# Performance work log

Hardware: AMD Instinct MI355X
Metric: run time of the kernel (lower is better)

## Reference

```python
import jax, jax.numpy as jnp
from jax import lax
import numpy as np

B, C, H, W = 16, 16, 256, 256
NOISE = 4
HID = 128
CDIM = 64
NCLS = 32
STEP_SIZE = 0.1
FIN = 3 * C + NOISE  # 52


def _lin(k, fin, fout, scale=None):
    # torch nn.Linear default init: U(-1/sqrt(fin), 1/sqrt(fin))
    s = (1.0 / np.sqrt(fin)) if scale is None else scale
    kw, kb = jax.random.split(k)
    w = jax.random.uniform(kw, (fin, fout), minval=-s, maxval=s, dtype=jnp.float32)
    b = jax.random.uniform(kb, (fout,), minval=-s, maxval=s, dtype=jnp.float32)
    return w, b


def setup_inputs() -> dict:
    key = jax.random.key(0)
    ks = jax.random.split(key, 8)
    x = jax.random.normal(ks[0], (B, C, H, W), dtype=jnp.float32)
    cond = jax.random.randint(ks[1], (B,), 0, NCLS)
    embed_tab = jax.random.normal(ks[2], (NCLS, CDIM), dtype=jnp.float32)
    film1_w, film1_b = _lin(ks[3], CDIM, 2 * HID)
    film2_w, film2_b = _lin(ks[4], CDIM, 2 * HID)
    fc1_w, fc1_b = _lin(ks[5], FIN, HID)
    fc2_w, fc2_b = _lin(ks[6], HID, HID)
    # original zero-inits fc3 (degenerate); use small random instead
    fc3_w, fc3_b = _lin(ks[7], HID, C, scale=0.02)
    return dict(x=x, cond=cond, embed_tab=embed_tab,
                film1_w=film1_w, film1_b=film1_b,
                film2_w=film2_w, film2_b=film2_b,
                fc1_w=fc1_w, fc1_b=fc1_b, fc2_w=fc2_w, fc2_b=fc2_b,
                fc3_w=fc3_w, fc3_b=fc3_b, n_steps=1)


def _dwconv(v, k2d):
    # depthwise 3x3 'same' conv, NCHW / OIHW
    kern = jnp.broadcast_to(k2d, (C, 1, 3, 3)).astype(v.dtype)
    return lax.conv_general_dilated(v, kern, (1, 1), 'SAME', feature_group_count=C)


def reference(x, cond, embed_tab, film1_w, film1_b, film2_w, film2_b,
              fc1_w, fc1_b, fc2_w, fc2_b, fc3_w, fc3_b, n_steps):
    sobel_x = jnp.array([[-1., 0., 1.], [-2., 0., 2.], [-1., 0., 1.]], jnp.float32)
    sobel_y = sobel_x.T
    emb = embed_tab[cond]                       # [B, CDIM]
    f1 = emb @ film1_w + film1_b                # [B, 2*HID]
    gamma1, beta1 = f1[:, :HID], f1[:, HID:]
    f2 = emb @ film2_w + film2_b
    gamma2, beta2 = f2[:, :HID], f2[:, HID:]
    for t in range(n_steps):
        gx = _dwconv(x, sobel_x)
        gy = _dwconv(x, sobel_y)
        noise = jax.random.normal(jax.random.fold_in(jax.random.key(1), t),
                                  (B, NOISE, H, W), dtype=x.dtype)
        feats = jnp.concatenate([x, gx, gy, noise], axis=1).transpose(0, 2, 3, 1)  # [B,H,W,FIN]
        h = jax.nn.relu(feats @ fc1_w + fc1_b)
        h = gamma1[:, None, None, :] * h + beta1[:, None, None, :]
        h = jax.nn.relu(h @ fc2_w + fc2_b)
        h = gamma2[:, None, None, :] * h + beta2[:, None, None, :]
        dx = (h @ fc3_w + fc3_b).transpose(0, 3, 1, 2)  # [B,C,H,W]
        dx = jnp.clip(dx, -10.0, 10.0)
        x = x + dx * STEP_SIZE
    return x
```

## Files before the change

### kernel.cpp

```cpp
#include <hip/hip_runtime.h>
#include <hip/hip_bf16.h>

using short8 = __attribute__((ext_vector_type(8))) short;
using f32x4  = __attribute__((ext_vector_type(4))) float;

constexpr int Bn = 16, Cc = 16, Hh = 256, Ww = 256;
constexpr int NOISEC = 4, HID = 128, CDIM = 64;
constexpr unsigned NTOT = (unsigned)Bn * NOISEC * Hh * Ww;
constexpr unsigned HALF = NTOT / 2;

__host__ __device__ __forceinline__ unsigned rotl(unsigned x, int d) {
    return (x << d) | (x >> (32 - d));
}

__host__ __device__ __forceinline__ void tf2x32(unsigned k0, unsigned k1,
                                                unsigned c0, unsigned c1,
                                                unsigned& o0, unsigned& o1) {
    unsigned k2 = k0 ^ k1 ^ 0x1BD11BDAu;
    unsigned x0 = c0 + k0, x1 = c1 + k1;
    x0 += x1; x1 = rotl(x1, 13); x1 ^= x0;
    x0 += x1; x1 = rotl(x1, 15); x1 ^= x0;
    x0 += x1; x1 = rotl(x1, 26); x1 ^= x0;
    x0 += x1; x1 = rotl(x1, 6);  x1 ^= x0;
    x0 += k1; x1 += k2 + 1u;
    x0 += x1; x1 = rotl(x1, 17); x1 ^= x0;
    x0 += x1; x1 = rotl(x1, 29); x1 ^= x0;
    x0 += x1; x1 = rotl(x1, 16); x1 ^= x0;
    x0 += x1; x1 = rotl(x1, 24); x1 ^= x0;
    x0 += k2; x1 += k0 + 2u;
    x0 += x1; x1 = rotl(x1, 13); x1 ^= x0;
    x0 += x1; x1 = rotl(x1, 15); x1 ^= x0;
    x0 += x1; x1 = rotl(x1, 26); x1 ^= x0;
    x0 += x1; x1 = rotl(x1, 6);  x1 ^= x0;
    x0 += k0; x1 += k1 + 3u;
    x0 += x1; x1 = rotl(x1, 17); x1 ^= x0;
    x0 += x1; x1 = rotl(x1, 29); x1 ^= x0;
    x0 += x1; x1 = rotl(x1, 16); x1 ^= x0;
    x0 += x1; x1 = rotl(x1, 24); x1 ^= x0;
    x0 += k1; x1 += k2 + 4u;
    x0 += x1; x1 = rotl(x1, 13); x1 ^= x0;
    x0 += x1; x1 = rotl(x1, 15); x1 ^= x0;
    x0 += x1; x1 = rotl(x1, 26); x1 ^= x0;
    x0 += x1; x1 = rotl(x1, 6);  x1 ^= x0;
    x0 += k2; x1 += k0 + 5u;
    o0 = x0; o1 = x1;
}

__device__ __forceinline__ float erfinv_f(float x) {
    float w = -log1pf(-x * x);
    float p;
    if (w < 5.0f) {
        w = w - 2.5f;
        p = 2.81022636e-08f;
        p = fmaf(p, w, 3.43273939e-07f);
        p = fmaf(p, w, -3.5233877e-06f);
        p = fmaf(p, w, -4.39150654e-06f);
        p = fmaf(p, w, 0.00021858087f);
        p = fmaf(p, w, -0.00125372503f);
        p = fmaf(p, w, -0.00417768164f);
        p = fmaf(p, w, 0.246640727f);
        p = fmaf(p, w, 1.50140941f);
    } else {
        w = sqrtf(w) - 3.0f;
        p = -0.000200214257f;
        p = fmaf(p, w, 0.000100950558f);
        p = fmaf(p, w, 0.00134934322f);
        p = fmaf(p, w, -0.00367342844f);
        p = fmaf(p, w, 0.00573950773f);
        p = fmaf(p, w, -0.0076224613f);
        p = fmaf(p, w, 0.00943887047f);
        p = fmaf(p, w, 1.00167406f);
        p = fmaf(p, w, 2.83297682f);
    }
    return p * x;
}

__device__ __forceinline__ float noise_val(unsigned j, unsigned fk0, unsigned fk1) {
    unsigned i = (j < HALF) ? j : (j - HALF);
    unsigned o0, o1;
    tf2x32(fk0, fk1, i, i + HALF, o0, o1);
    unsigned bits = (j < HALF) ? o0 : o1;
    unsigned fb = (bits >> 9) | 0x3F800000u;
    float f = __uint_as_float(fb) - 1.0f;
    const float lo = -0.99999994f;
    float u = f * 2.0f + lo;
    u = fmaxf(lo, u);
    return 1.4142135381698608f * erfinv_f(u);
}

__device__ __forceinline__ ushort f2bf(float f) {
    unsigned u = __float_as_uint(f);
    unsigned r = (u + 0x7FFFu + ((u >> 16) & 1u)) >> 16;
    return (ushort)r;
}

__device__ __forceinline__ unsigned cvtpk(float lo, float hi) {
    unsigned r;
    asm volatile("v_cvt_pk_bf16_f32 %0, %1, %2" : "=v"(r) : "v"(lo), "v"(hi));
    return r;
}

__device__ __forceinline__ unsigned rsw(int row) {
    return ((unsigned)((row ^ (row >> 4)) & 15)) << 4;
}

__global__ void film_kernel(const int* __restrict__ cond,
                            const float* __restrict__ embed,
                            const float* __restrict__ f1w, const float* __restrict__ f1b,
                            const float* __restrict__ f2w, const float* __restrict__ f2b,
                            float* __restrict__ film) {
    int b = blockIdx.x;
    int j = threadIdx.x;
    __shared__ float emb[CDIM];
    if (j < CDIM) emb[j] = embed[(size_t)cond[b] * CDIM + j];
    __syncthreads();
    float a1 = f1b[j], a2 = f2b[j];
    for (int c = 0; c < CDIM; ++c) {
        float e = emb[c];
        a1 += e * f1w[c * 2 * HID + j];
        a2 += e * f2w[c * 2 * HID + j];
    }
    int which = j >> 7;
    int idx = j & 127;
    float* fb_ = film + (size_t)b * 4 * HID;
    fb_[which * HID + idx] = a1;
    fb_[(2 + which) * HID + idx] = a2;
}

__global__ void prep_weights(const float* __restrict__ fc1w,
                             const float* __restrict__ fc2w,
                             const float* __restrict__ fc3w,
                             ushort* __restrict__ w1t, ushort* __restrict__ w2t,
                             ushort* __restrict__ w3t) {
    int i = blockIdx.x * 256 + threadIdx.x;
    if (i < 128 * 64) {
        int j = i >> 6, k = i & 63;
        w1t[i] = (k < 52) ? f2bf(fc1w[k * HID + j]) : (ushort)0;
    } else if (i < 8192 + 128 * 128) {
        int m = i - 8192;
        int j = m >> 7, k = m & 127;
        w2t[m] = f2bf(fc2w[k * HID + j]);
    } else if (i < 8192 + 16384 + 16 * 128) {
        int m = i - 24576;
        int c = m >> 7, k = m & 127;
        w3t[m] = f2bf(fc3w[k * Cc + c]);
    }
}

__global__ __launch_bounds__(256, 2)
void nca_mfma(const float* __restrict__ x,
              const ushort* __restrict__ w1t, const ushort* __restrict__ w2t,
              const ushort* __restrict__ w3t,
              const float* __restrict__ fc1b, const float* __restrict__ fc2b,
              const float* __restrict__ fc3b, const float* __restrict__ film,
              float* __restrict__ out, unsigned fk0, unsigned fk1) {
    __shared__ __align__(16) unsigned char Hb[256 * 256];

    const int P = blockIdx.x;
    const int blk = ((P & 7) << 9) | (P >> 3);
    const int b = blk >> 8, y = blk & 255;
    const int t = threadIdx.x;
    const float* xb = x + (size_t)b * Cc * Hh * Ww;

    {
        const int q  = t & 63;
        const int cq = t >> 6;
        const int px0 = q * 4;
        const bool okm = (y > 0), okp = (y < Hh - 1);
        const bool ql = (q > 0), qr = (q < 63);
        const float4 fz = {0.f, 0.f, 0.f, 0.f};

        float4 RM[4], RC[4], RP[4];
        #pragma unroll
        for (int cc = 0; cc < 4; ++cc) {
            const int c = cq * 4 + cc;
            const float* base = xb + ((size_t)c * Hh + (size_t)y) * Ww + px0;
            RM[cc] = okm ? *(const float4*)(base - Ww) : fz;
            RC[cc] = *(const float4*)(base);
            RP[cc] = okp ? *(const float4*)(base + Ww) : fz;
        }

        ushort nzs[4];
        {
            unsigned nbase = (((unsigned)(b * NOISEC + cq) * Hh + (unsigned)y) * Ww)
                             + (unsigned)px0;
            #pragma unroll
            for (int i = 0; i < 4; ++i)
                nzs[i] = f2bf(noise_val(nbase + (unsigned)i, fk0, fk1));
        }
        #pragma unroll
        for (int i = 0; i < 4; ++i) {
            const int row = px0 + i;
            const unsigned sw = rsw(row);
            *(ushort*)(Hb + row * 256 + (((224u ^ sw) + 2u * cq))) = nzs[i];
        }
        if (cq == 0) {
            #pragma unroll
            for (int i = 0; i < 4; ++i) {
                const int row = px0 + i;
                const unsigned sw = rsw(row);
                *(uint2*)(Hb + row * 256 + ((232u & 15u) + (224u ^ sw))) = (uint2){0u, 0u};
                *(uint4*)(Hb + row * 256 + (240u ^ sw)) = (uint4){0u, 0u, 0u, 0u};
            }
        }

        float vx[4][4], vgx[4][4], vgy[4][4];
        #pragma unroll
        for (int cc = 0; cc < 4; ++cc) {
            float4 rm = RM[cc], rc = RC[cc], rp = RP[cc];
            float mL = __shfl_up(rm.w, 1),  mR = __shfl_down(rm.x, 1);
            float cL = __shfl_up(rc.w, 1),  cR = __shfl_down(rc.x, 1);
            float pL = __shfl_up(rp.w, 1),  pR = __shfl_down(rp.x, 1);
            if (!ql) { mL = 0.f; cL = 0.f; pL = 0.f; }
            if (!qr) { mR = 0.f; cR = 0.f; pR = 0.f; }
            float am[6] = {mL, rm.x, rm.y, rm.z, rm.w, mR};
            float ac[6] = {cL, rc.x, rc.y, rc.z, rc.w, cR};
            float ap[6] = {pL, rp.x, rp.y, rp.z, rp.w, pR};
            #pragma unroll
            for (int i = 0; i < 4; ++i) {
                float a0 = am[i], a1 = am[i + 1], a2 = am[i + 2];
                float b0 = ac[i], b1 = ac[i + 1], b2 = ac[i + 2];
                float e0 = ap[i], e1 = ap[i + 1], e2 = ap[i + 2];
                vx[cc][i]  = b1;
                vgx[cc][i] = (a2 + 2.f * b2 + e2) - (a0 + 2.f * b0 + e0);
                vgy[cc][i] = (e0 + 2.f * e1 + e2) - (a0 + 2.f * a1 + a2);
            }
        }
        #pragma unroll
        for (int i = 0; i < 4; ++i) {
            const int row = px0 + i;
            const unsigned sw = rsw(row);
            unsigned char* rowp = Hb + row * 256;
            uint2 u;
            u.x = cvtpk(vx[0][i], vx[1][i]);  u.y = cvtpk(vx[2][i], vx[3][i]);
            *(uint2*)(rowp + ((128u + 8u * cq) ^ sw)) = u;
            u.x = cvtpk(vgx[0][i], vgx[1][i]); u.y = cvtpk(vgx[2][i], vgx[3][i]);
            *(uint2*)(rowp + ((160u + 8u * cq) ^ sw)) = u;
            u.x = cvtpk(vgy[0][i], vgy[1][i]); u.y = cvtpk(vgy[2][i], vgy[3][i]);
            *(uint2*)(rowp + ((192u + 8u * cq) ^ sw)) = u;
        }
    }
    __syncthreads();

    const int lane = t & 63, wv = t >> 6;
    const int q = lane >> 4, p = lane & 15;
    const int nt0 = wv * 4;

    unsigned swn[4];
    #pragma unroll
    for (int n = 0; n < 4; ++n) swn[n] = rsw((nt0 + n) * 16 + p);

    f32x4 acc[8][4];

    #pragma unroll
    for (int m = 0; m < 8; ++m)
        #pragma unroll
        for (int n = 0; n < 4; ++n) acc[m][n] = (f32x4){0.f, 0.f, 0.f, 0.f};

    #pragma unroll
    for (int ks = 0; ks < 2; ++ks) {
        short8 Bf[4];
        #pragma unroll
        for (int n = 0; n < 4; ++n) {
            int row = (nt0 + n) * 16 + p;
            Bf[n] = *(const short8*)(Hb + row * 256 +
                                     (((unsigned)(128 + ks * 64 + q * 16)) ^ swn[n]));
        }
        #pragma unroll
        for (int m = 0; m < 8; ++m) {
            short8 Af = *(const short8*)((const unsigned char*)w1t +
                                         (m * 16 + p) * 128 + ks * 64 + q * 16);
            #pragma unroll
            for (int n = 0; n < 4; ++n)
                acc[m][n] = __builtin_amdgcn_mfma_f32_16x16x32_bf16(Af, Bf[n], acc[m][n], 0, 0, 0);
        }
    }
    const float* flm = film + (size_t)b * 4 * HID;
    #pragma unroll
    for (int m = 0; m < 8; ++m) {
        int j0 = m * 16 + q * 4;
        float4 cb = *(const float4*)(fc1b + j0);
        float4 G  = *(const float4*)(flm + 0 * HID + j0);
        float4 Be = *(const float4*)(flm + 1 * HID + j0);
        #pragma unroll
        for (int n = 0; n < 4; ++n) {
            int row = (nt0 + n) * 16 + p;
            f32x4 a = acc[m][n];
            float v0 = G.x * fmaxf(a[0] + cb.x, 0.f) + Be.x;
            float v1 = G.y * fmaxf(a[1] + cb.y, 0.f) + Be.y;
            float v2 = G.z * fmaxf(a[2] + cb.z, 0.f) + Be.z;
            float v3 = G.w * fmaxf(a[3] + cb.w, 0.f) + Be.w;
            uint2 u2; u2.x = cvtpk(v0, v1); u2.y = cvtpk(v2, v3);
            *(uint2*)(Hb + row * 256 + (((unsigned)(m * 32 + q * 8)) ^ swn[n])) = u2;
        }
    }

    #pragma unroll
    for (int m = 0; m < 8; ++m)
        #pragma unroll
        for (int n = 0; n < 4; ++n) acc[m][n] = (f32x4){0.f, 0.f, 0.f, 0.f};

    #pragma unroll
    for (int ks = 0; ks < 4; ++ks) {
        short8 Bf[4];
        #pragma unroll
        for (int n = 0; n < 4; ++n) {
            int row = (nt0 + n) * 16 + p;
            Bf[n] = *(const short8*)(Hb + row * 256 +
                                     (((unsigned)(ks * 64 + q * 16)) ^ swn[n]));
        }
        #pragma unroll
        for (int m = 0; m < 8; ++m) {
            short8 Af = *(const short8*)((const unsigned char*)w2t +
                                         (m * 16 + p) * 256 + ks * 64 + q * 16);
            #pragma unroll
            for (int n = 0; n < 4; ++n)
                acc[m][n] = __builtin_amdgcn_mfma_f32_16x16x32_bf16(Af, Bf[n], acc[m][n], 0, 0, 0);
        }
    }
    #pragma unroll
    for (int m = 0; m < 8; ++m) {
        int j0 = m * 16 + q * 4;
        float4 cb = *(const float4*)(fc2b + j0);
        float4 G  = *(const float4*)(flm + 2 * HID + j0);
        float4 Be = *(const float4*)(flm + 3 * HID + j0);
        #pragma unroll
        for (int n = 0; n < 4; ++n) {
            int row = (nt0 + n) * 16 + p;
            f32x4 a = acc[m][n];
            float v0 = G.x * fmaxf(a[0] + cb.x, 0.f) + Be.x;
            float v1 = G.y * fmaxf(a[1] + cb.y, 0.f) + Be.y;
            float v2 = G.z * fmaxf(a[2] + cb.z, 0.f) + Be.z;
            float v3 = G.w * fmaxf(a[3] + cb.w, 0.f) + Be.w;
            uint2 u2; u2.x = cvtpk(v0, v1); u2.y = cvtpk(v2, v3);
            *(uint2*)(Hb + row * 256 + (((unsigned)(m * 32 + q * 8)) ^ swn[n])) = u2;
        }
    }

    float xpre[4][4];
    #pragma unroll
    for (int n = 0; n < 4; ++n) {
        int px = (nt0 + n) * 16 + p;
        #pragma unroll
        for (int r = 0; r < 4; ++r) {
            int c = q * 4 + r;
            xpre[n][r] = xb[(size_t)c * Hh * Ww + (size_t)y * Ww + px];
        }
    }

    f32x4 a3[4];
    #pragma unroll
    for (int n = 0; n < 4; ++n) a3[n] = (f32x4){0.f, 0.f, 0.f, 0.f};

    #pragma unroll
    for (int ks = 0; ks < 4; ++ks) {
        short8 Af = *(const short8*)((const unsigned char*)w3t +
                                     p * 256 + ks * 64 + q * 16);
        #pragma unroll
        for (int n = 0; n < 4; ++n) {
            int row = (nt0 + n) * 16 + p;
            short8 Bf = *(const short8*)(Hb + row * 256 +
                                         (((unsigned)(ks * 64 + q * 16)) ^ swn[n]));
            a3[n] = __builtin_amdgcn_mfma_f32_16x16x32_bf16(Af, Bf, a3[n], 0, 0, 0);
        }
    }
    {
        float4 c3 = *(const float4*)(fc3b + q * 4);
        float c3a[4] = {c3.x, c3.y, c3.z, c3.w};
        float* ob = out + (size_t)b * Cc * Hh * Ww;
        #pragma unroll
        for (int n = 0; n < 4; ++n) {
            int px = (nt0 + n) * 16 + p;
            #pragma unroll
            for (int r = 0; r < 4; ++r) {
                int c = q * 4 + r;
                float dx = a3[n][r] + c3a[r];
                dx = fminf(fmaxf(dx, -10.0f), 10.0f);
                size_t off = (size_t)c * Hh * Ww + (size_t)y * Ww + px;
                ob[off] = xpre[n][r] + 0.1f * dx;
            }
        }
    }
}

extern "C" void kernel_launch(void* const* d_in, const int* in_sizes, int n_in,
                              void* d_out, int out_size, void* d_ws, size_t ws_size,
                              hipStream_t stream) {
    const float* x     = (const float*)d_in[0];
    const int*   cond  = (const int*)d_in[1];
    const float* embed = (const float*)d_in[2];
    const float* f1w   = (const float*)d_in[3];
    const float* f1b   = (const float*)d_in[4];
    const float* f2w   = (const float*)d_in[5];
    const float* f2b   = (const float*)d_in[6];
    const float* fc1w  = (const float*)d_in[7];
    const float* fc1b  = (const float*)d_in[8];
    const float* fc2w  = (const float*)d_in[9];
    const float* fc2b  = (const float*)d_in[10];
    const float* fc3w  = (const float*)d_in[11];
    const float* fc3b  = (const float*)d_in[12];
    float* out = (float*)d_out;

    float*  film = (float*)d_ws;
    ushort* w1t  = (ushort*)((char*)d_ws + 32768);
    ushort* w2t  = (ushort*)((char*)d_ws + 32768 + 16384);
    ushort* w3t  = (ushort*)((char*)d_ws + 32768 + 16384 + 32768);

    unsigned fk0, fk1;
    tf2x32(0u, 1u, 0u, 0u, fk0, fk1);

    film_kernel<<<Bn, 256, 0, stream>>>(cond, embed, f1w, f1b, f2w, f2b, film);
    prep_weights<<<(8192 + 16384 + 2048 + 255) / 256, 256, 0, stream>>>(
        fc1w, fc2w, fc3w, w1t, w2t, w3t);
    nca_mfma<<<Bn * Hh, 256, 0, stream>>>(x, w1t, w2t, w3t, fc1b, fc2b, fc3b,
                                          film, out, fk0, fk1);
}
```

Baseline: 182.9 us.

## Make feature staging wave-local to drop block barrier, raise MFMA priority

The feature-building phase is remapped so each wave computes features for the same 64 pixels it later consumes in the MFMA stages. Because no wave then reads LDS rows written by another wave, the block-wide barrier is replaced by a local LDS wait. Horizontal halo values at the edges of each 16-lane group now come from extra scalar global loads instead of shuffles. The MFMA loops are also wrapped in s_setprio raises so matrix work gets issue priority over other waves' memory and elementwise phases. The cost is a few extra uncoalesced halo loads per wave.

```diff
diff --git a/kernel.cpp b/kernel.cpp
--- a/kernel.cpp
+++ b/kernel.cpp
@@ -160,14 +160,14 @@
     const int blk = ((P & 7) << 9) | (P >> 3);
     const int b = blk >> 8, y = blk & 255;
     const int t = threadIdx.x;
+    const int lane = t & 63, wv = t >> 6;
     const float* xb = x + (size_t)b * Cc * Hh * Ww;
 
     {
-        const int q  = t & 63;
-        const int cq = t >> 6;
-        const int px0 = q * 4;
+        const int pi = lane & 15;
+        const int cq = lane >> 4;
+        const int px0 = wv * 64 + pi * 4;
         const bool okm = (y > 0), okp = (y < Hh - 1);
-        const bool ql = (q > 0), qr = (q < 63);
         const float4 fz = {0.f, 0.f, 0.f, 0.f};
 
         float4 RM[4], RC[4], RP[4];
@@ -207,12 +207,26 @@
         float vx[4][4], vgx[4][4], vgy[4][4];
         #pragma unroll
         for (int cc = 0; cc < 4; ++cc) {
+            const int c = cq * 4 + cc;
+            const float* base = xb + ((size_t)c * Hh + (size_t)y) * Ww + px0;
             float4 rm = RM[cc], rc = RC[cc], rp = RP[cc];
             float mL = __shfl_up(rm.w, 1),  mR = __shfl_down(rm.x, 1);
             float cL = __shfl_up(rc.w, 1),  cR = __shfl_down(rc.x, 1);
             float pL = __shfl_up(rp.w, 1),  pR = __shfl_down(rp.x, 1);
-            if (!ql) { mL = 0.f; cL = 0.f; pL = 0.f; }
-            if (!qr) { mR = 0.f; cR = 0.f; pR = 0.f; }
+            if (pi == 0) {
+                if (px0 > 0) {
+                    mL = okm ? base[-Ww - 1] : 0.f;
+                    cL = base[-1];
+                    pL = okp ? base[Ww - 1] : 0.f;
+                } else { mL = 0.f; cL = 0.f; pL = 0.f; }
+            }
+            if (pi == 15) {
+                if (px0 + 4 < Ww) {
+                    mR = okm ? base[-Ww + 4] : 0.f;
+                    cR = base[4];
+                    pR = okp ? base[Ww + 4] : 0.f;
+                } else { mR = 0.f; cR = 0.f; pR = 0.f; }
+            }
             float am[6] = {mL, rm.x, rm.y, rm.z, rm.w, mR};
             float ac[6] = {cL, rc.x, rc.y, rc.z, rc.w, cR};
             float ap[6] = {pL, rp.x, rp.y, rp.z, rp.w, pR};
@@ -240,9 +254,8 @@
             *(uint2*)(rowp + ((192u + 8u * cq) ^ sw)) = u;
         }
     }
-    __syncthreads();
-
-    const int lane = t & 63, wv = t >> 6;
+    asm volatile("s_waitcnt lgkmcnt(0)" ::: "memory");
+
     const int q = lane >> 4, p = lane & 15;
     const int nt0 = wv * 4;
 
@@ -257,6 +270,7 @@
         #pragma unroll
         for (int n = 0; n < 4; ++n) acc[m][n] = (f32x4){0.f, 0.f, 0.f, 0.f};
 
+    __builtin_amdgcn_s_setprio(1);
     #pragma unroll
     for (int ks = 0; ks < 2; ++ks) {
         short8 Bf[4];
@@ -275,6 +289,7 @@
                 acc[m][n] = __builtin_amdgcn_mfma_f32_16x16x32_bf16(Af, Bf[n], acc[m][n], 0, 0, 0);
         }
     }
+    __builtin_amdgcn_s_setprio(0);
     const float* flm = film + (size_t)b * 4 * HID;
     #pragma unroll
     for (int m = 0; m < 8; ++m) {
@@ -300,6 +315,7 @@
         #pragma unroll
         for (int n = 0; n < 4; ++n) acc[m][n] = (f32x4){0.f, 0.f, 0.f, 0.f};
 
+    __builtin_amdgcn_s_setprio(1);
     #pragma unroll
     for (int ks = 0; ks < 4; ++ks) {
         short8 Bf[4];
@@ -318,6 +334,7 @@
                 acc[m][n] = __builtin_amdgcn_mfma_f32_16x16x32_bf16(Af, Bf[n], acc[m][n], 0, 0, 0);
         }
     }
+    __builtin_amdgcn_s_setprio(0);
     #pragma unroll
     for (int m = 0; m < 8; ++m) {
         int j0 = m * 16 + q * 4;
@@ -352,6 +369,7 @@
     #pragma unroll
     for (int n = 0; n < 4; ++n) a3[n] = (f32x4){0.f, 0.f, 0.f, 0.f};
 
+    __builtin_amdgcn_s_setprio(1);
     #pragma unroll
     for (int ks = 0; ks < 4; ++ks) {
         short8 Af = *(const short8*)((const unsigned char*)w3t +
@@ -364,6 +382,7 @@
             a3[n] = __builtin_amdgcn_mfma_f32_16x16x32_bf16(Af, Bf, a3[n], 0, 0, 0);
         }
     }
+    __builtin_amdgcn_s_setprio(0);
     {
         float4 c3 = *(const float4*)(fc3b + q * 4);
         float c3a[4] = {c3.x, c3.y, c3.z, c3.w};
```

New measurement: 184.5 us. Within noise of the previous version (+0.9%).
